# Optimization experiments

Measured on AMD Instinct MI355X. Metric: run time of the kernel, lower is better.

The kernel has to match this reference:

```python
import jax, jax.numpy as jnp
import numpy as np

L = 4


def make_coord(h, w):
    # pixel-center coords in [-1,1], shape (h*w, 2), dim order (y, x)
    ys = -1.0 + 1.0 / h + (2.0 / h) * jnp.arange(h, dtype=jnp.float32)
    xs = -1.0 + 1.0 / w + (2.0 / w) * jnp.arange(w, dtype=jnp.float32)
    gy, gx = jnp.meshgrid(ys, xs, indexing='ij')
    return jnp.stack([gy, gx], axis=-1).reshape(-1, 2)


def bilinear_sample(feat, gx, gy):
    # feat: (B,C,H,W); gx,gy in [-1,1], shape (B,N); align_corners=True
    B, C, H, W = feat.shape
    ix = (gx + 1.0) * 0.5 * (W - 1)
    iy = (gy + 1.0) * 0.5 * (H - 1)
    x0f = jnp.floor(ix)
    y0f = jnp.floor(iy)
    x0 = jnp.clip(x0f.astype(jnp.int32), 0, W - 1)
    x1 = jnp.clip(x0 + 1, 0, W - 1)
    y0 = jnp.clip(y0f.astype(jnp.int32), 0, H - 1)
    y1 = jnp.clip(y0 + 1, 0, H - 1)
    wx1 = ix - x0f
    wx0 = 1.0 - wx1
    wy1 = iy - y0f
    wy0 = 1.0 - wy1
    featf = feat.reshape(B, C, H * W)

    def g(yi, xi):
        idx = yi * W + xi  # (B,N)
        return jnp.take_along_axis(featf, idx[:, None, :], axis=2)  # (B,C,N)

    out = (g(y0, x0) * (wy0 * wx0)[:, None, :] + g(y0, x1) * (wy0 * wx1)[:, None, :]
           + g(y1, x0) * (wy1 * wx0)[:, None, :] + g(y1, x1) * (wy1 * wx1)[:, None, :])
    return out.transpose(0, 2, 1)  # (B,N,C)


def pos_enc(x):
    # x: (B,N,2) -> (B,N,4L); per dim: [sin_0..sin_{L-1}, cos_0..cos_{L-1}]
    freq = (2.0 ** jnp.arange(L, dtype=jnp.float32)) * np.pi
    spec = x[..., None] * freq  # (B,N,2,L)
    enc = jnp.concatenate([jnp.sin(spec), jnp.cos(spec)], axis=-1)  # (B,N,2,2L)
    return enc.reshape(*x.shape[:-1], 4 * L)


def mlp(x, w0, b0, w1, b1, w2, b2, w3, b3):
    h = jax.nn.relu(x @ w0 + b0)
    h = jax.nn.relu(h @ w1 + b1)
    h = jax.nn.relu(h @ w2 + b2)
    return h @ w3 + b3


def setup_inputs() -> dict:
    key = jax.random.key(0)
    ks = jax.random.split(key, 8)
    B, C, H, W = 4, 64, 128, 128
    hid, out_dim = 256, 3
    in_dim = C + 2 + 4 * L + 2  # 84
    s = 0.05
    return {
        'inp': jax.random.normal(ks[0], (B, C, H, W), jnp.float32),
        'w0': jax.random.normal(ks[1], (in_dim, hid), jnp.float32) * s,
        'b0': jnp.zeros((hid,), jnp.float32),
        'w1': jax.random.normal(ks[2], (hid, hid), jnp.float32) * s,
        'b1': jnp.zeros((hid,), jnp.float32),
        'w2': jax.random.normal(ks[3], (hid, hid), jnp.float32) * s,
        'b2': jnp.zeros((hid,), jnp.float32),
        'w3': jax.random.normal(ks[4], (hid, out_dim), jnp.float32) * s,
        'b3': jnp.zeros((out_dim,), jnp.float32),
        'scale': 2,
    }


def reference(inp, w0, b0, w1, b1, w2, b2, w3, b3, scale):
    B, C, H, W = inp.shape
    th, tw = int(round(H * scale)), int(round(W * scale))
    N = th * tw
    coord = jnp.broadcast_to(make_coord(th, tw)[None], (B, N, 2))
    # cell = (2/th, 2/tw); rel_cell = cell * (H, W)
    rel_cell = jnp.broadcast_to(
        jnp.array([2.0 / th * H, 2.0 / tw * W], jnp.float32), (B, N, 2))
    # feature-pixel coordinate map, appended as extra channels so one gather serves both
    fc = make_coord(H, W).reshape(H, W, 2).transpose(2, 0, 1)  # (2,H,W)
    aug = jnp.concatenate([inp, jnp.broadcast_to(fc[None], (B, 2, H, W))], axis=1)

    pe = pos_enc(coord)  # same for all 4 ensemble branches
    hw_scale = jnp.array([H, W], jnp.float32)
    rx, ry = 1.0 / H, 1.0 / W
    eps = 1e-6

    preds, areas = [], []
    for vx in (-1, 1):
        for vy in (-1, 1):
            c0 = jnp.clip(coord[..., 0] + vx * rx + eps, -1 + 1e-6, 1 - 1e-6)
            c1 = jnp.clip(coord[..., 1] + vy * ry + eps, -1 + 1e-6, 1 - 1e-6)
            # grid_sample uses (x, y) = flipped coord -> gx=c1, gy=c0
            q = bilinear_sample(aug, c1, c0)  # (B,N,C+2)
            q_feat, q_coord = q[..., :C], q[..., C:]
            rel = (coord - q_coord) * hw_scale  # (B,N,2)
            x = jnp.concatenate([q_feat, rel, pe, rel_cell], axis=-1)
            preds.append(mlp(x, w0, b0, w1, b1, w2, b2, w3, b3))
            areas.append(jnp.abs(rel[..., 0] * rel[..., 1]) + 1e-9)

    areas = [areas[3], areas[2], areas[1], areas[0]]  # diagonal swap
    tot = areas[0] + areas[1] + areas[2] + areas[3]
    ret = sum(p * (a / tot)[..., None] for p, a in zip(preds, areas))  # (B,N,out)
    return ret.reshape(B, th, tw, -1).transpose(0, 3, 1, 2)  # (B,out,th,tw)
```

## Files before the change

kernel.cpp:

```cpp
#include <hip/hip_runtime.h>
#include <math.h>

#define NB 4
#define NH 128
#define NW 128
#define TH 256
#define TW 256
#define K0 96
#define MROWS 128
#define PIXB 32

typedef _Float16 f16;
typedef f16  f16x8 __attribute__((ext_vector_type(8)));
typedef f16  f16x4v __attribute__((ext_vector_type(4)));
typedef float f32x4 __attribute__((ext_vector_type(4)));
typedef float f32x16 __attribute__((ext_vector_type(16)));

#define OFF_W1 24576
#define OFF_W2 (OFF_W1 + 65536)
#define OFF_W3 (OFF_W2 + 65536)
#define OFF_PE (OFF_W3 + 4096)
#define WS_W_ELEMS (OFF_PE + 4096)
#define FT_ELEMS (NB * NH * NW * 64)

__device__ __forceinline__ int act_off(int row, int colByte) {
  return row * 512 + (colByte ^ ((row & 31) << 4));
}

__global__ void cvt_weights(const float* __restrict__ w0, const float* __restrict__ w1,
                            const float* __restrict__ w2, const float* __restrict__ w3,
                            f16* __restrict__ ws) {
  const int i = blockIdx.x * 256 + threadIdx.x;
  if (i < 24576) {
    const int n = i / 96, k = i - n * 96;
    ws[i] = (k < 84) ? (f16)w0[k * 256 + n] : (f16)0.f;
  } else if (i < OFF_W2) {
    const int j = i - OFF_W1; const int n = j >> 8, k = j & 255;
    ws[i] = (f16)w1[k * 256 + n];
  } else if (i < OFF_W3) {
    const int j = i - OFF_W2; const int n = j >> 8, k = j & 255;
    ws[i] = (f16)w2[k * 256 + n];
  } else if (i < OFF_PE) {
    const int j = i - OFF_W3; const int n = j >> 8, k = j & 255;
    ws[i] = (n < 3) ? (f16)w3[k * 3 + n] : (f16)0.f;
  } else if (i < WS_W_ELEMS) {
    const int j = i - OFF_PE;
    const int o = (j & 2047) >> 3, e = j & 7;
    const float c = (2.0f * o + 1.0f) / 256.0f - 1.0f;
    const float f = (float)(1 << (e & 3)) * (float)M_PI;
    ws[i] = (f16)((e < 4) ? sinf(c * f) : cosf(c * f));
  }
}

__global__ void transpose_feat(const float* __restrict__ feat, f16* __restrict__ ft) {
  __shared__ f16 tile[64][66];
  const int bid = blockIdx.x;
  const int xt = bid & 1, y = (bid >> 1) & 127, b = bid >> 8;
  const int x0 = xt * 64;
  {
    const int c4 = threadIdx.x >> 6, x = threadIdx.x & 63;
#pragma unroll
    for (int co = 0; co < 16; ++co) {
      const int c = co * 4 + c4;
      tile[x][c] = (f16)feat[((size_t)(b * 64 + c) * NH + y) * NW + x0 + x];
    }
  }
  __syncthreads();
  {
    const int x4 = threadIdx.x >> 6, c = threadIdx.x & 63;
#pragma unroll
    for (int xo = 0; xo < 16; ++xo) {
      const int x = xo * 4 + x4;
      ft[((size_t)(b * NH + y) * NW + x0 + x) * 64 + c] = tile[x][c];
    }
  }
}

template<int K>
__device__ __forceinline__ void dense_layer(const f16* __restrict__ Wt,
                                            const float* __restrict__ bias,
                                            char* actc, int w, int l) {
  constexpr int NK = K / 16;
  constexpr int CH = (NK < 8) ? NK : 8;
  const int lo = l & 31, hi = l >> 5;
  const f16* wsrc = Wt + (size_t)(w * 64 + lo) * K + hi * 8;

  f32x16 acc[4][2];
#pragma unroll
  for (int nt = 0; nt < 2; ++nt) {
    f32x16 ci;
#pragma unroll
    for (int g = 0; g < 4; ++g) {
      const float4 b4 = *(const float4*)(bias + w * 64 + nt * 32 + 8 * g + 4 * hi);
      ci[4 * g + 0] = b4.x; ci[4 * g + 1] = b4.y; ci[4 * g + 2] = b4.z; ci[4 * g + 3] = b4.w;
    }
#pragma unroll
    for (int mt = 0; mt < 4; ++mt) acc[mt][nt] = ci;
  }

  f16x8 Bb[2][4];
#pragma unroll
  for (int mt = 0; mt < 4; ++mt)
    Bb[0][mt] = *(const f16x8*)(actc + act_off(mt * 32 + lo, hi * 16));

#pragma unroll
  for (int c = 0; c < NK; c += CH) {
    f16x8 Wr[CH][2];
#pragma unroll
    for (int kk = 0; kk < CH; ++kk) {
      Wr[kk][0] = *(const f16x8*)(wsrc + 0 * 32 * K + (c + kk) * 16);
      Wr[kk][1] = *(const f16x8*)(wsrc + (size_t)1 * 32 * K + (c + kk) * 16);
    }
#pragma unroll
    for (int kk = 0; kk < CH; ++kk) {
      const int ks = c + kk;
      if (ks + 1 < NK) {
#pragma unroll
        for (int mt = 0; mt < 4; ++mt)
          Bb[(ks + 1) & 1][mt] =
              *(const f16x8*)(actc + act_off(mt * 32 + lo, (ks + 1) * 32 + hi * 16));
        asm volatile("s_waitcnt lgkmcnt(4)" ::: "memory");
      } else {
        asm volatile("s_waitcnt lgkmcnt(0)" ::: "memory");
      }
      __builtin_amdgcn_sched_barrier(0);

      __builtin_amdgcn_s_setprio(1);
#pragma unroll
      for (int mt = 0; mt < 4; ++mt) {
        acc[mt][0] = __builtin_amdgcn_mfma_f32_32x32x16_f16(Wr[kk][0], Bb[ks & 1][mt], acc[mt][0], 0, 0, 0);
        acc[mt][1] = __builtin_amdgcn_mfma_f32_32x32x16_f16(Wr[kk][1], Bb[ks & 1][mt], acc[mt][1], 0, 0, 0);
      }
      __builtin_amdgcn_s_setprio(0);
    }
  }

  __syncthreads();

#pragma unroll
  for (int mt = 0; mt < 4; ++mt)
#pragma unroll
    for (int nt = 0; nt < 2; ++nt)
#pragma unroll
      for (int g = 0; g < 4; ++g) {
        f16x4v o;
        o[0] = (f16)fmaxf(acc[mt][nt][4 * g + 0], 0.f);
        o[1] = (f16)fmaxf(acc[mt][nt][4 * g + 1], 0.f);
        o[2] = (f16)fmaxf(acc[mt][nt][4 * g + 2], 0.f);
        o[3] = (f16)fmaxf(acc[mt][nt][4 * g + 3], 0.f);
        const int row = mt * 32 + lo;
        const int colB = w * 128 + nt * 64 + 16 * g + 8 * hi;
        *(f16x4v*)(actc + act_off(row, colB)) = o;
      }
}

template<bool USE_FT>
__global__ __launch_bounds__(256, 2) void inr2d_mfma(
    const float* __restrict__ feat, const f16* __restrict__ ft,
    const float* __restrict__ b0, const float* __restrict__ b1,
    const float* __restrict__ b2, const float* __restrict__ b3,
    const f16* __restrict__ ws, float* __restrict__ out)
{
  __shared__ f16 act[MROWS * 256];
  __shared__ f16 pred_s[MROWS][4];

  char* actc = (char*)act;
  const int t = threadIdx.x;
  const int blk = ((blockIdx.x & 7) << 10) | (blockIdx.x >> 3);

  {
    const int r = t >> 1, sub = t & 1;
    const int pix = r >> 2, e = r & 3;
    const int gp = blk * PIXB + pix;
    const int b = gp >> 16, rem = gp & 65535;
    const int oy = rem >> 8, ox = rem & 255;

    const float cy = (2.0f * oy + 1.0f) / (float)TH - 1.0f;
    const float cx = (2.0f * ox + 1.0f) / (float)TW - 1.0f;
    const float vx = (e & 2) ? 1.0f : -1.0f;
    const float vy = (e & 1) ? 1.0f : -1.0f;
    const float rr = 1.0f / (float)NH;

    float c0 = fminf(fmaxf(cy + vx * rr + 1e-6f, -1.0f + 1e-6f), 1.0f - 1e-6f);
    float c1 = fminf(fmaxf(cx + vy * rr + 1e-6f, -1.0f + 1e-6f), 1.0f - 1e-6f);

    const float ix = (c1 + 1.0f) * 0.5f * (float)(NW - 1);
    const float iy = (c0 + 1.0f) * 0.5f * (float)(NH - 1);
    const float x0f = floorf(ix), y0f = floorf(iy);
    int x0 = (int)x0f; x0 = max(0, min(x0, NW - 1));
    int x1 = min(x0 + 1, NW - 1);
    int y0 = (int)y0f; y0 = max(0, min(y0, NH - 1));
    int y1 = min(y0 + 1, NH - 1);
    const float wx1 = ix - x0f, wx0 = 1.0f - wx1;
    const float wy1 = iy - y0f, wy0 = 1.0f - wy1;
    const float w00 = wy0 * wx0, w01 = wy0 * wx1, w10 = wy1 * wx0, w11 = wy1 * wx1;

    if (USE_FT) {
      const f16* fb = ft + (size_t)b * (NH * NW * 64);
      const f16* r00 = fb + (size_t)(y0 * NW + x0) * 64 + sub * 32;
      const f16* r01 = fb + (size_t)(y0 * NW + x1) * 64 + sub * 32;
      const f16* r10 = fb + (size_t)(y1 * NW + x0) * 64 + sub * 32;
      const f16* r11 = fb + (size_t)(y1 * NW + x1) * 64 + sub * 32;
#pragma unroll
      for (int h = 0; h < 4; ++h) {
        const f16x8 a00 = *(const f16x8*)(r00 + h * 8);
        const f16x8 a01 = *(const f16x8*)(r01 + h * 8);
        const f16x8 a10 = *(const f16x8*)(r10 + h * 8);
        const f16x8 a11 = *(const f16x8*)(r11 + h * 8);
        f16x8 o;
#pragma unroll
        for (int i = 0; i < 8; ++i) {
          o[i] = (f16)(w00 * (float)a00[i] + w01 * (float)a01[i] +
                       w10 * (float)a10[i] + w11 * (float)a11[i]);
        }
        *(f16x8*)(actc + act_off(r, 64 * sub + 16 * h)) = o;
      }
    } else {
      const float* fb = feat + (size_t)b * 64 * NH * NW;
      const int i00 = y0 * NW + x0, i01 = y0 * NW + x1;
      const int i10 = y1 * NW + x0, i11 = y1 * NW + x1;
#pragma unroll
      for (int i = 0; i < 32; ++i) {
        const int c = sub * 32 + i;
        const float* fc = fb + (size_t)c * (NH * NW);
        const float v = w00 * fc[i00] + w01 * fc[i01] + w10 * fc[i10] + w11 * fc[i11];
        *(f16*)(actc + act_off(r, 2 * c)) = (f16)v;
      }
    }
    if (sub == 0) {
      const float qy = -1.0f + 1.0f / NH + (2.0f / NH) * (wy0 * (float)y0 + wy1 * (float)y1);
      const float qx = -1.0f + 1.0f / NW + (2.0f / NW) * (wx0 * (float)x0 + wx1 * (float)x1);
      const float rely = (cy - qy) * (float)NH;
      const float relx = (cx - qx) * (float)NW;
      *(f16*)(actc + act_off(r, 2 * 64)) = (f16)rely;
      *(f16*)(actc + act_off(r, 2 * 65)) = (f16)relx;
      if (USE_FT) {
        const f16* py = ws + OFF_PE + (size_t)oy * 8;
        const f16* px = ws + OFF_PE + 2048 + (size_t)ox * 8;
#pragma unroll
        for (int j = 0; j < 8; ++j) {
          *(f16*)(actc + act_off(r, 2 * (66 + j))) = py[j];
          *(f16*)(actc + act_off(r, 2 * (74 + j))) = px[j];
        }
      } else {
#pragma unroll
        for (int ll = 0; ll < 4; ++ll) {
          const float f = (float)(1 << ll) * (float)M_PI;
          *(f16*)(actc + act_off(r, 2 * (66 + ll))) = (f16)sinf(cy * f);
          *(f16*)(actc + act_off(r, 2 * (70 + ll))) = (f16)cosf(cy * f);
          *(f16*)(actc + act_off(r, 2 * (74 + ll))) = (f16)sinf(cx * f);
          *(f16*)(actc + act_off(r, 2 * (78 + ll))) = (f16)cosf(cx * f);
        }
      }
      *(f16*)(actc + act_off(r, 2 * 82)) = (f16)1.0f;
      *(f16*)(actc + act_off(r, 2 * 83)) = (f16)1.0f;
#pragma unroll
      for (int z = 84; z < K0; ++z) *(f16*)(actc + act_off(r, 2 * z)) = (f16)0.f;
    }
  }
  __syncthreads();

  const int w = t >> 6, l = t & 63;

  dense_layer<K0 >(ws,          b0, actc, w, l);
  __syncthreads();
  dense_layer<256>(ws + OFF_W1, b1, actc, w, l);
  __syncthreads();
  dense_layer<256>(ws + OFF_W2, b2, actc, w, l);
  __syncthreads();

  {
    const int nl = l & 15, kq = l >> 4;
    const f16* Abase = ws + OFF_W3 + nl * 256 + kq * 8;
#pragma unroll
    for (int p = 0; p < 2; ++p) {
      const int row = w * 32 + p * 16 + nl;
      f32x4 acc = {0.f, 0.f, 0.f, 0.f};
#pragma unroll
      for (int ks = 0; ks < 8; ++ks) {
        f16x8 a = *(const f16x8*)(Abase + ks * 32);
        f16x8 b = *(const f16x8*)(actc + act_off(row, 64 * ks + 16 * kq));
        acc = __builtin_amdgcn_mfma_f32_16x16x32_f16(a, b, acc, 0, 0, 0);
      }
      if (l < 16) {
        f16x4v pr;
        pr[0] = (f16)(acc[0] + b3[0]); pr[1] = (f16)(acc[1] + b3[1]);
        pr[2] = (f16)(acc[2] + b3[2]); pr[3] = (f16)0.f;
        *(f16x4v*)(&pred_s[w * 32 + p * 16 + l][0]) = pr;
      }
    }
  }
  __syncthreads();

  if (t < PIXB * 3) {
    const int pix = t / 3, o = t - pix * 3;
    const int gp = blk * PIXB + pix;
    const int b = gp >> 16, rem = gp & 65535;
    const int oy = rem >> 8, ox = rem & 255;
    const float cy = (2.0f * oy + 1.0f) / (float)TH - 1.0f;
    const float cx = (2.0f * ox + 1.0f) / (float)TW - 1.0f;
    const float rr = 1.0f / (float)NH;
    float ar[4];
#pragma unroll
    for (int e = 0; e < 4; ++e) {
      const float vx = (e & 2) ? 1.0f : -1.0f;
      const float vy = (e & 1) ? 1.0f : -1.0f;
      float c0 = fminf(fmaxf(cy + vx * rr + 1e-6f, -1.0f + 1e-6f), 1.0f - 1e-6f);
      float c1 = fminf(fmaxf(cx + vy * rr + 1e-6f, -1.0f + 1e-6f), 1.0f - 1e-6f);
      const float ix = (c1 + 1.0f) * 0.5f * (float)(NW - 1);
      const float iy = (c0 + 1.0f) * 0.5f * (float)(NH - 1);
      const float x0f = floorf(ix), y0f = floorf(iy);
      int x0 = (int)x0f; x0 = max(0, min(x0, NW - 1));
      int x1 = min(x0 + 1, NW - 1);
      int y0 = (int)y0f; y0 = max(0, min(y0, NH - 1));
      int y1 = min(y0 + 1, NH - 1);
      const float wx1 = ix - x0f, wx0 = 1.0f - wx1;
      const float wy1 = iy - y0f, wy0 = 1.0f - wy1;
      const float qy = -1.0f + 1.0f / NH + (2.0f / NH) * (wy0 * (float)y0 + wy1 * (float)y1);
      const float qx = -1.0f + 1.0f / NW + (2.0f / NW) * (wx0 * (float)x0 + wx1 * (float)x1);
      const float rely = (cy - qy) * (float)NH;
      const float relx = (cx - qx) * (float)NW;
      ar[e] = fabsf(rely * relx) + 1e-9f;
    }
    const int r0 = pix * 4;
    const float tot = ar[0] + ar[1] + ar[2] + ar[3];
    const float v = (float)pred_s[r0][o] * ar[3] + (float)pred_s[r0 + 1][o] * ar[2] +
                    (float)pred_s[r0 + 2][o] * ar[1] + (float)pred_s[r0 + 3][o] * ar[0];
    out[(((size_t)b * 3 + o) << 16) + (oy << 8) + ox] = v / tot;
  }
}

extern "C" void kernel_launch(void* const* d_in, const int* in_sizes, int n_in,
                              void* d_out, int out_size, void* d_ws, size_t ws_size,
                              hipStream_t stream) {
  const float* feat = (const float*)d_in[0];
  const float* w0 = (const float*)d_in[1];
  const float* b0 = (const float*)d_in[2];
  const float* w1 = (const float*)d_in[3];
  const float* b1 = (const float*)d_in[4];
  const float* w2 = (const float*)d_in[5];
  const float* b2 = (const float*)d_in[6];
  const float* w3 = (const float*)d_in[7];
  const float* b3 = (const float*)d_in[8];
  float* out = (float*)d_out;
  f16* ws = (f16*)d_ws;

  cvt_weights<<<(WS_W_ELEMS + 255) / 256, 256, 0, stream>>>(w0, w1, w2, w3, ws);

  const int blocks = (NB * TH * TW) / PIXB;
  const bool use_ft = ws_size >= (size_t)(WS_W_ELEMS + FT_ELEMS) * sizeof(f16);
  if (use_ft) {
    f16* ft = ws + WS_W_ELEMS;
    transpose_feat<<<NB * NH * (NW / 64), 256, 0, stream>>>(feat, ft);
    inr2d_mfma<true><<<blocks, 256, 0, stream>>>(feat, ft, b0, b1, b2, b3, ws, out);
  } else {
    inr2d_mfma<false><<<blocks, 256, 0, stream>>>(feat, nullptr, b0, b1, b2, b3, ws, out);
  }
}
```

Measured before the change: 412.6 us.

## Keep MLP activations in registers per wave, converting accumulators via lane shuffles

The hidden layers are restructured so each wave owns 32 rows and computes all 256 output columns, holding activations in registers instead of round-tripping through LDS between layers. Accumulator outputs are packed to f16 and rearranged into the next layer's B-operand layout with cross-half-wave shuffles, removing LDS writes/reads and block barriers between layers. The cost is that each wave now streams the full weight matrix from global/L2 (4x more weight traffic per block) and register pressure rises sharply (8 f32x16 accumulators plus 16 f16x8 operands), which may cause spills or lower occupancy under launch_bounds(256,2).

```diff
diff --git a/kernel.cpp b/kernel.cpp
--- a/kernel.cpp
+++ b/kernel.cpp
@@ -9,10 +9,12 @@
 #define K0 96
 #define MROWS 128
 #define PIXB 32
+#define SST 104
 
 typedef _Float16 f16;
 typedef f16  f16x8 __attribute__((ext_vector_type(8)));
 typedef f16  f16x4v __attribute__((ext_vector_type(4)));
+typedef __fp16 fp16x2 __attribute__((ext_vector_type(2)));
 typedef float f32x4 __attribute__((ext_vector_type(4)));
 typedef float f32x16 __attribute__((ext_vector_type(16)));
 
@@ -76,82 +78,79 @@
   }
 }
 
+__device__ __forceinline__ int pk(float a, float b) {
+  fp16x2 h = __builtin_amdgcn_cvt_pkrtz(fmaxf(a, 0.f), fmaxf(b, 0.f));
+  return __builtin_bit_cast(int, h);
+}
+
+__device__ __forceinline__ void transition(const f32x16* acc, f16x8* Bn, bool hiL) {
+#pragma unroll
+  for (int nt = 0; nt < 8; ++nt) {
+    const f32x16 a = acc[nt];
+    int X0 = pk(a[0], a[1]),  X1 = pk(a[2], a[3]);
+    int Y0 = pk(a[4], a[5]),  Y1 = pk(a[6], a[7]);
+    int pX0 = __shfl_xor(X0, 32), pX1 = __shfl_xor(X1, 32);
+    int pY0 = __shfl_xor(Y0, 32), pY1 = __shfl_xor(Y1, 32);
+    int4 q0;
+    q0.x = hiL ? pY0 : X0;
+    q0.y = hiL ? pY1 : X1;
+    q0.z = hiL ? Y0 : pX0;
+    q0.w = hiL ? Y1 : pX1;
+    Bn[2 * nt] = __builtin_bit_cast(f16x8, q0);
+    int X2 = pk(a[8], a[9]),   X3 = pk(a[10], a[11]);
+    int Y2 = pk(a[12], a[13]), Y3 = pk(a[14], a[15]);
+    int pX2 = __shfl_xor(X2, 32), pX3 = __shfl_xor(X3, 32);
+    int pY2 = __shfl_xor(Y2, 32), pY3 = __shfl_xor(Y3, 32);
+    int4 q1;
+    q1.x = hiL ? pY2 : X2;
+    q1.y = hiL ? pY3 : X3;
+    q1.z = hiL ? Y2 : pX2;
+    q1.w = hiL ? Y3 : pX3;
+    Bn[2 * nt + 1] = __builtin_bit_cast(f16x8, q1);
+  }
+}
+
 template<int K>
-__device__ __forceinline__ void dense_layer(const f16* __restrict__ Wt,
-                                            const float* __restrict__ bias,
-                                            char* actc, int w, int l) {
+__device__ __forceinline__ void dense_reg(const f16* __restrict__ Wt,
+                                          const float* __restrict__ bias,
+                                          const f16x8* Bf, f32x16* acc, int l) {
   constexpr int NK = K / 16;
-  constexpr int CH = (NK < 8) ? NK : 8;
   const int lo = l & 31, hi = l >> 5;
-  const f16* wsrc = Wt + (size_t)(w * 64 + lo) * K + hi * 8;
-
-  f32x16 acc[4][2];
-#pragma unroll
-  for (int nt = 0; nt < 2; ++nt) {
+#pragma unroll
+  for (int nt = 0; nt < 8; ++nt) {
     f32x16 ci;
 #pragma unroll
     for (int g = 0; g < 4; ++g) {
-      const float4 b4 = *(const float4*)(bias + w * 64 + nt * 32 + 8 * g + 4 * hi);
+      const float4 b4 = *(const float4*)(bias + nt * 32 + 8 * g + 4 * hi);
       ci[4 * g + 0] = b4.x; ci[4 * g + 1] = b4.y; ci[4 * g + 2] = b4.z; ci[4 * g + 3] = b4.w;
     }
-#pragma unroll
-    for (int mt = 0; mt < 4; ++mt) acc[mt][nt] = ci;
-  }
-
-  f16x8 Bb[2][4];
-#pragma unroll
-  for (int mt = 0; mt < 4; ++mt)
-    Bb[0][mt] = *(const f16x8*)(actc + act_off(mt * 32 + lo, hi * 16));
-
-#pragma unroll
-  for (int c = 0; c < NK; c += CH) {
-    f16x8 Wr[CH][2];
-#pragma unroll
-    for (int kk = 0; kk < CH; ++kk) {
-      Wr[kk][0] = *(const f16x8*)(wsrc + 0 * 32 * K + (c + kk) * 16);
-      Wr[kk][1] = *(const f16x8*)(wsrc + (size_t)1 * 32 * K + (c + kk) * 16);
-    }
-#pragma unroll
-    for (int kk = 0; kk < CH; ++kk) {
-      const int ks = c + kk;
-      if (ks + 1 < NK) {
-#pragma unroll
-        for (int mt = 0; mt < 4; ++mt)
-          Bb[(ks + 1) & 1][mt] =
-              *(const f16x8*)(actc + act_off(mt * 32 + lo, (ks + 1) * 32 + hi * 16));
-        asm volatile("s_waitcnt lgkmcnt(4)" ::: "memory");
-      } else {
-        asm volatile("s_waitcnt lgkmcnt(0)" ::: "memory");
-      }
-      __builtin_amdgcn_sched_barrier(0);
-
-      __builtin_amdgcn_s_setprio(1);
-#pragma unroll
-      for (int mt = 0; mt < 4; ++mt) {
-        acc[mt][0] = __builtin_amdgcn_mfma_f32_32x32x16_f16(Wr[kk][0], Bb[ks & 1][mt], acc[mt][0], 0, 0, 0);
-        acc[mt][1] = __builtin_amdgcn_mfma_f32_32x32x16_f16(Wr[kk][1], Bb[ks & 1][mt], acc[mt][1], 0, 0, 0);
-      }
-      __builtin_amdgcn_s_setprio(0);
-    }
-  }
-
-  __syncthreads();
-
-#pragma unroll
-  for (int mt = 0; mt < 4; ++mt)
-#pragma unroll
-    for (int nt = 0; nt < 2; ++nt)
-#pragma unroll
-      for (int g = 0; g < 4; ++g) {
-        f16x4v o;
-        o[0] = (f16)fmaxf(acc[mt][nt][4 * g + 0], 0.f);
-        o[1] = (f16)fmaxf(acc[mt][nt][4 * g + 1], 0.f);
-        o[2] = (f16)fmaxf(acc[mt][nt][4 * g + 2], 0.f);
-        o[3] = (f16)fmaxf(acc[mt][nt][4 * g + 3], 0.f);
-        const int row = mt * 32 + lo;
-        const int colB = w * 128 + nt * 64 + 16 * g + 8 * hi;
-        *(f16x4v*)(actc + act_off(row, colB)) = o;
-      }
+    acc[nt] = ci;
+  }
+  const f16* wsrc = Wt + (size_t)lo * K + hi * 8;
+  f16x8 Wr0[4], Wr1[4];
+#pragma unroll
+  for (int i = 0; i < 4; ++i) Wr0[i] = *(const f16x8*)(wsrc + (size_t)i * 32 * K);
+#pragma unroll
+  for (int ks = 0; ks < NK; ++ks) {
+#pragma unroll
+    for (int i = 0; i < 4; ++i)
+      Wr1[i] = *(const f16x8*)(wsrc + (size_t)(4 + i) * 32 * K + ks * 16);
+    __builtin_amdgcn_s_setprio(1);
+#pragma unroll
+    for (int i = 0; i < 4; ++i)
+      acc[i] = __builtin_amdgcn_mfma_f32_32x32x16_f16(Wr0[i], Bf[ks], acc[i], 0, 0, 0);
+    __builtin_amdgcn_s_setprio(0);
+    if (ks + 1 < NK) {
+#pragma unroll
+      for (int i = 0; i < 4; ++i)
+        Wr0[i] = *(const f16x8*)(wsrc + (size_t)i * 32 * K + (ks + 1) * 16);
+    }
+    __builtin_amdgcn_s_setprio(1);
+#pragma unroll
+    for (int i = 0; i < 4; ++i)
+      acc[4 + i] = __builtin_amdgcn_mfma_f32_32x32x16_f16(Wr1[i], Bf[ks], acc[4 + i], 0, 0, 0);
+    __builtin_amdgcn_s_setprio(0);
+  }
 }
 
 template<bool USE_FT>
@@ -165,6 +164,7 @@
   __shared__ f16 pred_s[MROWS][4];
 
   char* actc = (char*)act;
+  f16* stage = act;
   const int t = threadIdx.x;
   const int blk = ((blockIdx.x & 7) << 10) | (blockIdx.x >> 3);
 
@@ -209,11 +209,10 @@
         const f16x8 a11 = *(const f16x8*)(r11 + h * 8);
         f16x8 o;
 #pragma unroll
-        for (int i = 0; i < 8; ++i) {
+        for (int i = 0; i < 8; ++i)
           o[i] = (f16)(w00 * (float)a00[i] + w01 * (float)a01[i] +
                        w10 * (float)a10[i] + w11 * (float)a11[i]);
-        }
-        *(f16x8*)(actc + act_off(r, 64 * sub + 16 * h)) = o;
+        *(f16x8*)(stage + r * SST + sub * 32 + h * 8) = o;
       }
     } else {
       const float* fb = feat + (size_t)b * 64 * NH * NW;
@@ -223,8 +222,8 @@
       for (int i = 0; i < 32; ++i) {
         const int c = sub * 32 + i;
         const float* fc = fb + (size_t)c * (NH * NW);
-        const float v = w00 * fc[i00] + w01 * fc[i01] + w10 * fc[i10] + w11 * fc[i11];
-        *(f16*)(actc + act_off(r, 2 * c)) = (f16)v;
+        stage[r * SST + c] = (f16)(w00 * fc[i00] + w01 * fc[i01] +
+                                   w10 * fc[i10] + w11 * fc[i11]);
       }
     }
     if (sub == 0) {
@@ -232,41 +231,64 @@
       const float qx = -1.0f + 1.0f / NW + (2.0f / NW) * (wx0 * (float)x0 + wx1 * (float)x1);
       const float rely = (cy - qy) * (float)NH;
       const float relx = (cx - qx) * (float)NW;
-      *(f16*)(actc + act_off(r, 2 * 64)) = (f16)rely;
-      *(f16*)(actc + act_off(r, 2 * 65)) = (f16)relx;
+      stage[r * SST + 64] = (f16)rely;
+      stage[r * SST + 65] = (f16)relx;
       if (USE_FT) {
         const f16* py = ws + OFF_PE + (size_t)oy * 8;
         const f16* px = ws + OFF_PE + 2048 + (size_t)ox * 8;
 #pragma unroll
         for (int j = 0; j < 8; ++j) {
-          *(f16*)(actc + act_off(r, 2 * (66 + j))) = py[j];
-          *(f16*)(actc + act_off(r, 2 * (74 + j))) = px[j];
+          stage[r * SST + 66 + j] = py[j];
+          stage[r * SST + 74 + j] = px[j];
         }
       } else {
 #pragma unroll
         for (int ll = 0; ll < 4; ++ll) {
           const float f = (float)(1 << ll) * (float)M_PI;
-          *(f16*)(actc + act_off(r, 2 * (66 + ll))) = (f16)sinf(cy * f);
-          *(f16*)(actc + act_off(r, 2 * (70 + ll))) = (f16)cosf(cy * f);
-          *(f16*)(actc + act_off(r, 2 * (74 + ll))) = (f16)sinf(cx * f);
-          *(f16*)(actc + act_off(r, 2 * (78 + ll))) = (f16)cosf(cx * f);
+          stage[r * SST + 66 + ll] = (f16)sinf(cy * f);
+          stage[r * SST + 70 + ll] = (f16)cosf(cy * f);
+          stage[r * SST + 74 + ll] = (f16)sinf(cx * f);
+          stage[r * SST + 78 + ll] = (f16)cosf(cx * f);
         }
       }
-      *(f16*)(actc + act_off(r, 2 * 82)) = (f16)1.0f;
-      *(f16*)(actc + act_off(r, 2 * 83)) = (f16)1.0f;
-#pragma unroll
-      for (int z = 84; z < K0; ++z) *(f16*)(actc + act_off(r, 2 * z)) = (f16)0.f;
+      stage[r * SST + 82] = (f16)1.0f;
+      stage[r * SST + 83] = (f16)1.0f;
+#pragma unroll
+      for (int z = 84; z < K0; ++z) stage[r * SST + z] = (f16)0.f;
     }
   }
   __syncthreads();
 
   const int w = t >> 6, l = t & 63;
-
-  dense_layer<K0 >(ws,          b0, actc, w, l);
-  __syncthreads();
-  dense_layer<256>(ws + OFF_W1, b1, actc, w, l);
-  __syncthreads();
-  dense_layer<256>(ws + OFF_W2, b2, actc, w, l);
+  const int lo = l & 31, hi = l >> 5;
+  const bool hiL = (hi != 0);
+
+  f16x8 B0[6];
+#pragma unroll
+  for (int ks = 0; ks < 6; ++ks)
+    B0[ks] = *(const f16x8*)(stage + (size_t)(w * 32 + lo) * SST + ks * 16 + hi * 8);
+  __syncthreads();
+
+  f32x16 acc[8];
+  f16x8 B1[16];
+
+  dense_reg<K0 >(ws,          b0, B0, acc, l);
+  transition(acc, B1, hiL);
+  dense_reg<256>(ws + OFF_W1, b1, B1, acc, l);
+  transition(acc, B1, hiL);
+  dense_reg<256>(ws + OFF_W2, b2, B1, acc, l);
+
+#pragma unroll
+  for (int nt = 0; nt < 8; ++nt)
+#pragma unroll
+    for (int g = 0; g < 4; ++g) {
+      f16x4v o;
+      o[0] = (f16)fmaxf(acc[nt][4 * g + 0], 0.f);
+      o[1] = (f16)fmaxf(acc[nt][4 * g + 1], 0.f);
+      o[2] = (f16)fmaxf(acc[nt][4 * g + 2], 0.f);
+      o[3] = (f16)fmaxf(acc[nt][4 * g + 3], 0.f);
+      *(f16x4v*)(actc + act_off(w * 32 + lo, nt * 64 + 16 * g + 8 * hi)) = o;
+    }
   __syncthreads();
 
   {
@@ -275,17 +297,17 @@
 #pragma unroll
     for (int p = 0; p < 2; ++p) {
       const int row = w * 32 + p * 16 + nl;
-      f32x4 acc = {0.f, 0.f, 0.f, 0.f};
+      f32x4 a4 = {0.f, 0.f, 0.f, 0.f};
 #pragma unroll
       for (int ks = 0; ks < 8; ++ks) {
         f16x8 a = *(const f16x8*)(Abase + ks * 32);
         f16x8 b = *(const f16x8*)(actc + act_off(row, 64 * ks + 16 * kq));
-        acc = __builtin_amdgcn_mfma_f32_16x16x32_f16(a, b, acc, 0, 0, 0);
+        a4 = __builtin_amdgcn_mfma_f32_16x16x32_f16(a, b, a4, 0, 0, 0);
       }
       if (l < 16) {
         f16x4v pr;
-        pr[0] = (f16)(acc[0] + b3[0]); pr[1] = (f16)(acc[1] + b3[1]);
-        pr[2] = (f16)(acc[2] + b3[2]); pr[3] = (f16)0.f;
+        pr[0] = (f16)(a4[0] + b3[0]); pr[1] = (f16)(a4[1] + b3[1]);
+        pr[2] = (f16)(a4[2] + b3[2]); pr[3] = (f16)0.f;
         *(f16x4v*)(&pred_s[w * 32 + p * 16 + l][0]) = pr;
       }
     }
```

Measured after the change: 1.147 ms. +178.1%, slower.

## Double-buffer weight register loads in dense layers and use packed f16 bilinear blend

Applied to the files above, without the earlier changes.

The dense layer now loads weights in chunks of four k-steps into two alternating register buffers, prefetching the next chunk while MFMAs consume the current one. Previously each chunk of up to eight k-steps was loaded and then consumed with no overlap. The bilinear gather also computes its blend directly in packed f16 vector arithmetic instead of converting to f32 and back. This lowers ALU work but accumulates in half precision and raises register pressure from the second weight buffer.

```diff
diff --git a/kernel.cpp b/kernel.cpp
--- a/kernel.cpp
+++ b/kernel.cpp
@@ -81,7 +81,7 @@
                                             const float* __restrict__ bias,
                                             char* actc, int w, int l) {
   constexpr int NK = K / 16;
-  constexpr int CH = (NK < 8) ? NK : 8;
+  constexpr int CH = 4;
   const int lo = l & 31, hi = l >> 5;
   const f16* wsrc = Wt + (size_t)(w * 64 + lo) * K + hi * 8;
 
@@ -98,6 +98,15 @@
     for (int mt = 0; mt < 4; ++mt) acc[mt][nt] = ci;
   }
 
+  f16x8 WA[CH][2], WB[CH][2];
+#pragma unroll
+  for (int kk = 0; kk < CH; ++kk) {
+    if (kk < NK) {
+      WA[kk][0] = *(const f16x8*)(wsrc + 0 * 32 * K + kk * 16);
+      WA[kk][1] = *(const f16x8*)(wsrc + (size_t)1 * 32 * K + kk * 16);
+    }
+  }
+
   f16x8 Bb[2][4];
 #pragma unroll
   for (int mt = 0; mt < 4; ++mt)
@@ -105,15 +114,21 @@
 
 #pragma unroll
   for (int c = 0; c < NK; c += CH) {
-    f16x8 Wr[CH][2];
-#pragma unroll
-    for (int kk = 0; kk < CH; ++kk) {
-      Wr[kk][0] = *(const f16x8*)(wsrc + 0 * 32 * K + (c + kk) * 16);
-      Wr[kk][1] = *(const f16x8*)(wsrc + (size_t)1 * 32 * K + (c + kk) * 16);
+    f16x8 (*Wcur)[2] = ((c / CH) & 1) ? WB : WA;
+    f16x8 (*Wnxt)[2] = ((c / CH) & 1) ? WA : WB;
+    if (c + CH < NK) {
+#pragma unroll
+      for (int kk = 0; kk < CH; ++kk) {
+        if (c + CH + kk < NK) {
+          Wnxt[kk][0] = *(const f16x8*)(wsrc + 0 * 32 * K + (c + CH + kk) * 16);
+          Wnxt[kk][1] = *(const f16x8*)(wsrc + (size_t)1 * 32 * K + (c + CH + kk) * 16);
+        }
+      }
     }
 #pragma unroll
     for (int kk = 0; kk < CH; ++kk) {
       const int ks = c + kk;
+      if (ks >= NK) continue;
       if (ks + 1 < NK) {
 #pragma unroll
         for (int mt = 0; mt < 4; ++mt)
@@ -128,8 +143,8 @@
       __builtin_amdgcn_s_setprio(1);
 #pragma unroll
       for (int mt = 0; mt < 4; ++mt) {
-        acc[mt][0] = __builtin_amdgcn_mfma_f32_32x32x16_f16(Wr[kk][0], Bb[ks & 1][mt], acc[mt][0], 0, 0, 0);
-        acc[mt][1] = __builtin_amdgcn_mfma_f32_32x32x16_f16(Wr[kk][1], Bb[ks & 1][mt], acc[mt][1], 0, 0, 0);
+        acc[mt][0] = __builtin_amdgcn_mfma_f32_32x32x16_f16(Wcur[kk][0], Bb[ks & 1][mt], acc[mt][0], 0, 0, 0);
+        acc[mt][1] = __builtin_amdgcn_mfma_f32_32x32x16_f16(Wcur[kk][1], Bb[ks & 1][mt], acc[mt][1], 0, 0, 0);
       }
       __builtin_amdgcn_s_setprio(0);
     }
@@ -196,6 +211,7 @@
     const float w00 = wy0 * wx0, w01 = wy0 * wx1, w10 = wy1 * wx0, w11 = wy1 * wx1;
 
     if (USE_FT) {
+      const f16 h00 = (f16)w00, h01 = (f16)w01, h10 = (f16)w10, h11 = (f16)w11;
       const f16* fb = ft + (size_t)b * (NH * NW * 64);
       const f16* r00 = fb + (size_t)(y0 * NW + x0) * 64 + sub * 32;
       const f16* r01 = fb + (size_t)(y0 * NW + x1) * 64 + sub * 32;
@@ -207,12 +223,7 @@
         const f16x8 a01 = *(const f16x8*)(r01 + h * 8);
         const f16x8 a10 = *(const f16x8*)(r10 + h * 8);
         const f16x8 a11 = *(const f16x8*)(r11 + h * 8);
-        f16x8 o;
-#pragma unroll
-        for (int i = 0; i < 8; ++i) {
-          o[i] = (f16)(w00 * (float)a00[i] + w01 * (float)a01[i] +
-                       w10 * (float)a10[i] + w11 * (float)a11[i]);
-        }
+        f16x8 o = a00 * h00 + a01 * h01 + a10 * h10 + a11 * h11;
         *(f16x8*)(actc + act_off(r, 64 * sub + 16 * h)) = o;
       }
     } else {
```

Measured after the change: 400.0 us. 1.03x faster.
